# Performance work log

Hardware: AMD Instinct MI355X
Metric: run time of the kernel (lower is better)

## Reference

```python
import jax, jax.numpy as jnp
import numpy as np

TWN_THRESHOLD_FACTOR = 0.05
BN_EPS = 1e-5


def ternary_quantize(w):
    # threshold = 0.05 * max|w| (detached); q in {-1, 0, +1}
    t = TWN_THRESHOLD_FACTOR * jnp.max(jnp.abs(jax.lax.stop_gradient(w)))
    return (w > t).astype(w.dtype) - (w < -t).astype(w.dtype)


def conv2d(x, w, b):
    q = ternary_quantize(w)
    y = jax.lax.conv_general_dilated(x, q, (1, 1), 'VALID',
                                     dimension_numbers=('NCHW', 'OIHW', 'NCHW'))
    return y + b[None, :, None, None]


def linear(x, w, b):
    q = ternary_quantize(w)
    return x @ q.T + b


def bn_train(x, gamma, beta, axes):
    # training-mode batch norm (biased variance), matches torch BN in train()
    mean = jnp.mean(x, axis=axes, keepdims=True)
    var = jnp.var(x, axis=axes, keepdims=True)
    xhat = (x - mean) * jax.lax.rsqrt(var + BN_EPS)
    shape = [1] * x.ndim
    shape[1] = x.shape[1]
    return xhat * gamma.reshape(shape) + beta.reshape(shape)


def maxpool2(x):
    return jax.lax.reduce_window(x, -jnp.inf, jax.lax.max,
                                 (1, 1, 2, 2), (1, 1, 2, 2), 'VALID')


def setup_inputs() -> dict:
    key = jax.random.key(0)
    ks = jax.random.split(key, 8)
    B, Cin, H, W = 512, 1, 28, 28
    C1, C2, K = 64, 128, 5
    FLAT, F1, F2 = 4 * 4 * C2, 512, 10
    inp = {
        'x': jax.random.normal(ks[0], (B, Cin, H, W), jnp.float32),
        'conv1_w': jax.random.normal(ks[1], (C1, Cin, K, K), jnp.float32) * (1.0 / np.sqrt(Cin * K * K)),
        'conv1_b': jax.random.normal(ks[2], (C1,), jnp.float32) * 0.05,
        'bn1_g': jnp.ones((C1,), jnp.float32),
        'bn1_b': jnp.zeros((C1,), jnp.float32),
        'conv2_w': jax.random.normal(ks[3], (C2, C1, K, K), jnp.float32) * (1.0 / np.sqrt(C1 * K * K)),
        'conv2_b': jax.random.normal(ks[4], (C2,), jnp.float32) * 0.05,
        'bn2_g': jnp.ones((C2,), jnp.float32),
        'bn2_b': jnp.zeros((C2,), jnp.float32),
        'fc1_w': jax.random.normal(ks[5], (F1, FLAT), jnp.float32) * (1.0 / np.sqrt(FLAT)),
        'fc1_b': jax.random.normal(ks[6], (F1,), jnp.float32) * 0.05,
        'bn3_g': jnp.ones((F1,), jnp.float32),
        'bn3_b': jnp.zeros((F1,), jnp.float32),
        'fc2_w': jax.random.normal(ks[7], (F2, F1), jnp.float32) * (1.0 / np.sqrt(F1)),
        'fc2_b': jnp.zeros((F2,), jnp.float32),
    }
    return inp


def reference(x, conv1_w, conv1_b, bn1_g, bn1_b, conv2_w, conv2_b, bn2_g, bn2_b,
              fc1_w, fc1_b, bn3_g, bn3_b, fc2_w, fc2_b):
    h = jax.nn.relu(bn_train(conv2d(x, conv1_w, conv1_b), bn1_g, bn1_b, (0, 2, 3)))
    h = maxpool2(h)  # [B, 64, 12, 12]
    h = jax.nn.relu(bn_train(conv2d(h, conv2_w, conv2_b), bn2_g, bn2_b, (0, 2, 3)))
    h = maxpool2(h)  # [B, 128, 4, 4]
    h = h.reshape(h.shape[0], -1)  # [B, 2048]
    h = jax.nn.relu(bn_train(linear(h, fc1_w, fc1_b), bn3_g, bn3_b, (0,)))
    return linear(h, fc2_w, fc2_b)  # [B, 10]
```

## Files before the change

### kernel.cpp

```cpp
#include <hip/hip_runtime.h>
#include <stdint.h>

#define EPS 1e-5f

typedef short v8s __attribute__((ext_vector_type(8)));
typedef float v4f __attribute__((ext_vector_type(4)));

static const size_t W1F  = 4096;
static const size_t W2F  = 8192;
static const size_t WF2F = 212992;
static const size_t A_F  = 262144;
static const size_t B_F  = 19136512;
static const size_t WF1T = B_F + 1048576;

__device__ inline unsigned short f2bf(float f) {
    unsigned u = __float_as_uint(f);
    return (unsigned short)((u + 0x7FFF + ((u >> 16) & 1)) >> 16);
}

__device__ __forceinline__ void stage16(const unsigned short* g, unsigned short* l) {
    __builtin_amdgcn_global_load_lds(
        (const __attribute__((address_space(1))) unsigned int*)g,
        (__attribute__((address_space(3))) unsigned int*)l, 16, 0, 0);
}

__global__ void k_zero(float* p, int n) {
    int i = blockIdx.x * blockDim.x + threadIdx.x;
    if (i < n) p[i] = 0.f;
}

__global__ void k_absmax4(const float* __restrict__ w0, int n0,
                          const float* __restrict__ w1, int n1,
                          const float* __restrict__ w2, int n2,
                          const float* __restrict__ w3, int n3,
                          float* outv) {
    int blk = blockIdx.x;
    const float* w; int n; unsigned* out; int nb; int bi;
    if (blk < 1)        { w = w0; n = n0; out = (unsigned*)(outv + 0); nb = 1;   bi = blk;      }
    else if (blk < 17)  { w = w1; n = n1; out = (unsigned*)(outv + 1); nb = 16;  bi = blk - 1;  }
    else if (blk < 209) { w = w2; n = n2; out = (unsigned*)(outv + 2); nb = 192; bi = blk - 17; }
    else                { w = w3; n = n3; out = (unsigned*)(outv + 3); nb = 1;   bi = blk - 209; }
    float m = 0.f;
    for (int i = bi * 256 + threadIdx.x; i < n; i += nb * 256)
        m = fmaxf(m, fabsf(w[i]));
    #pragma unroll
    for (int o = 32; o; o >>= 1) m = fmaxf(m, __shfl_down(m, o));
    if ((threadIdx.x & 63) == 0) atomicMax(out, __float_as_uint(m));
}

__global__ void k_quantE(const float* __restrict__ c1w, const float* __restrict__ c2w,
                         const float* __restrict__ f2w, const float* __restrict__ am,
                         float* __restrict__ w1t, unsigned short* __restrict__ w2u,
                         float* __restrict__ wf2) {
    int blk = blockIdx.x;
    if (blk < 1) {
        float t = 0.05f * am[0];
        for (int i = threadIdx.x; i < 1600; i += 256) {
            float v = c1w[i];
            float q = (float)((v > t) - (v < -t));
            int c = i / 25, k = i - c * 25;
            w1t[k * 64 + c] = q;
        }
    } else if (blk < 401) {
        float t = 0.05f * am[1];
        int base = (blk - 1) * 512;
        #pragma unroll
        for (int jj = 0; jj < 2; ++jj) {
            int i = base + jj * 256 + threadIdx.x;
            int j    = i & 7;
            int lane = (i >> 3) & 63;
            int mt   = (i >> 9) & 7;
            int ks   = (i >> 12) & 1;
            int p    = i >> 13;
            int c  = mt * 16 + (lane & 15);
            int ci = ks * 32 + (lane >> 4) * 8 + j;
            float v = c2w[c * 1600 + ci * 25 + p];
            w2u[i] = (v > t) ? (unsigned short)0x3F80
                             : ((v < -t) ? (unsigned short)0xBF80 : (unsigned short)0);
        }
    } else {
        float t = 0.05f * am[3];
        for (int i = threadIdx.x; i < 5120; i += 256) {
            float v = f2w[i];
            wf2[i] = (float)((v > t) - (v < -t));
        }
    }
}

__global__ __launch_bounds__(512) void k_conv1(const float* __restrict__ x,
                                               const float* __restrict__ w1t,
                                               unsigned* __restrict__ pmn1,
                                               float* __restrict__ sum,
                                               float* __restrict__ ssq) {
    __shared__ float xs[784];
    __shared__ float red[2][8][64];
    int b = blockIdx.x;
    const float4* xim = (const float4*)(x + (size_t)b * 784);
    for (int i = threadIdx.x; i < 196; i += 512) ((float4*)xs)[i] = xim[i];
    int c  = threadIdx.x & 63;
    int wv = threadIdx.x >> 6;
    float w[25];
    #pragma unroll
    for (int k = 0; k < 25; ++k) w[k] = w1t[k * 64 + c];
    __syncthreads();
    unsigned* ob = pmn1 + (size_t)b * 9216;
    float s = 0.f, s2 = 0.f;
    int ph = 0, pw = wv;
    for (int it = 0; it < 18; ++it) {
        const float* xp = xs + (ph * 2) * 28 + pw * 2;
        float win[36];
        #pragma unroll
        for (int i = 0; i < 6; ++i)
            #pragma unroll
            for (int j = 0; j < 3; ++j) {
                float2 t2 = *(const float2*)(xp + i * 28 + j * 2);
                win[i * 6 + j * 2] = t2.x; win[i * 6 + j * 2 + 1] = t2.y;
            }
        float v00 = 0.f, v01 = 0.f, v10 = 0.f, v11 = 0.f;
        #pragma unroll
        for (int i = 0; i < 5; ++i)
            #pragma unroll
            for (int j = 0; j < 5; ++j) {
                float wk = w[i * 5 + j];
                v00 = fmaf(win[i * 6 + j],           wk, v00);
                v01 = fmaf(win[i * 6 + j + 1],       wk, v01);
                v10 = fmaf(win[(i + 1) * 6 + j],     wk, v10);
                v11 = fmaf(win[(i + 1) * 6 + j + 1], wk, v11);
            }
        s  += v00 + v01 + v10 + v11;
        s2 += v00 * v00 + v01 * v01 + v10 * v10 + v11 * v11;
        float mx = fmaxf(fmaxf(v00, v01), fmaxf(v10, v11));
        float mn = fminf(fminf(v00, v01), fminf(v10, v11));
        ob[(ph * 12 + pw) * 64 + c] = ((unsigned)f2bf(mx) << 16) | (unsigned)f2bf(mn);
        pw += 8; if (pw >= 12) { pw -= 12; ++ph; }
    }
    red[0][wv][c] = s; red[1][wv][c] = s2;
    __syncthreads();
    if (threadIdx.x < 64) {
        float S = 0.f, S2 = 0.f;
        #pragma unroll
        for (int i = 0; i < 8; ++i) { S += red[0][i][threadIdx.x]; S2 += red[1][i][threadIdx.x]; }
        atomicAdd(&sum[threadIdx.x], S);
        atomicAdd(&ssq[threadIdx.x], S2);
    }
}

__global__ void k_bnpool1(const unsigned* __restrict__ pmn1,
                          const float* __restrict__ c1sum, const float* __restrict__ c1ssq,
                          const float* __restrict__ g1, const float* __restrict__ b1,
                          unsigned short* __restrict__ pool1) {
    int i = blockIdx.x * 256 + threadIdx.x;
    int c = i & 63;
    const float invN = 1.f / 294912.f;
    float mean = c1sum[c] * invN;
    float var  = c1ssq[c] * invN - mean * mean;
    float sc = g1[c] * rsqrtf(var + EPS);
    float sh = b1[c] - mean * sc;
    unsigned u = pmn1[i];
    float mx = __uint_as_float(u & 0xffff0000u);
    float mn = __uint_as_float(u << 16);
    float v = (sc > 0.f) ? mx : mn;
    pool1[i] = f2bf(fmaxf(0.f, fmaf(v, sc, sh)));
}

__global__ __launch_bounds__(256) void k_conv2(const unsigned short* __restrict__ pool1,
                                               const unsigned short* __restrict__ wfrag,
                                               float* __restrict__ pmn,
                                               float* __restrict__ sum,
                                               float* __restrict__ ssq) {
    __shared__ unsigned short xs[144 * 76];
    __shared__ unsigned short wb[2][4096];
    __shared__ float reds[2][64], redq[2][64];
    int b     = blockIdx.x >> 1;
    int mhalf = blockIdx.x & 1;
    int tid  = threadIdx.x;
    int lane = tid & 63;
    int wave = tid >> 6;
    int nh = wave & 1, kp = wave >> 1;
    const unsigned short* src = pool1 + (size_t)b * 9216;
    for (int i = tid; i < 1152; i += 256) {
        int r = i >> 3, part = i & 7;
        *(float4*)(&xs[r * 76 + part * 8]) = *(const float4*)(src + r * 64 + part * 8);
    }
    #pragma unroll
    for (int h = 0; h < 2; ++h) {
        int ksm = wave * 2 + h;
        int ks = ksm >> 2, mt = ksm & 3;
        const unsigned short* g = wfrag + (size_t)(ks * 8 + mhalf * 4 + mt) * 512 + lane * 8;
        stage16(g, &wb[0][ks * 2048 + mt * 512 + lane * 8]);
    }
    __syncthreads();

    int n = lane & 15, quad = lane >> 4;
    int ow = n & 7;
    int ohb0 = nh * 4 + (n >> 3);
    int col0 = kp * 32 + quad * 8;
    v4f acc[4][2];
    #pragma unroll
    for (int mm = 0; mm < 4; ++mm) { acc[mm][0] = (v4f){0,0,0,0}; acc[mm][1] = (v4f){0,0,0,0}; }
    for (int p = 0; p < 25; ++p) {
        int cur = p & 1;
        if (p < 24) {
            #pragma unroll
            for (int h = 0; h < 2; ++h) {
                int ksm = wave * 2 + h;
                int ks = ksm >> 2, mt = ksm & 3;
                const unsigned short* g = wfrag +
                    (size_t)(((p + 1) * 2 + ks) * 8 + mhalf * 4 + mt) * 512 + lane * 8;
                stage16(g, &wb[cur ^ 1][ks * 2048 + mt * 512 + lane * 8]);
            }
        }
        int kh = p / 5, kw = p - (p / 5) * 5;
        int col = (ow + kw) * 76 + col0;
        v8s bf0 = *(const v8s*)(&xs[(ohb0 + kh) * 912 + col]);
        v8s bf1 = *(const v8s*)(&xs[(ohb0 + 2 + kh) * 912 + col]);
        #pragma unroll
        for (int mm = 0; mm < 4; ++mm) {
            v8s af = *(const v8s*)(&wb[cur][kp * 2048 + mm * 512 + lane * 8]);
            acc[mm][0] = __builtin_amdgcn_mfma_f32_16x16x32_bf16(af, bf0, acc[mm][0], 0, 0, 0);
            acc[mm][1] = __builtin_amdgcn_mfma_f32_16x16x32_bf16(af, bf1, acc[mm][1], 0, 0, 0);
        }
        __syncthreads();
    }
    float* mbuf = (float*)xs;
    if (kp == 1) {
        float* d = mbuf + (nh * 64 + lane) * 36;
        #pragma unroll
        for (int mm = 0; mm < 4; ++mm) {
            *(v4f*)(d + mm * 8)     = acc[mm][0];
            *(v4f*)(d + mm * 8 + 4) = acc[mm][1];
        }
    }
    __syncthreads();
    if (kp == 0) {
        const float* s = mbuf + (nh * 64 + lane) * 36;
        #pragma unroll
        for (int mm = 0; mm < 4; ++mm) {
            acc[mm][0] += *(const v4f*)(s + mm * 8);
            acc[mm][1] += *(const v4f*)(s + mm * 8 + 4);
        }
        float* po = pmn + (size_t)b * 4096;
        #pragma unroll
        for (int mm = 0; mm < 4; ++mm) {
            int cl0 = mm * 16 + quad * 4;
            #pragma unroll
            for (int r = 0; r < 4; ++r) {
                int cl = cl0 + r;
                int c  = mhalf * 64 + cl;
                float sA = 0.f, s2A = 0.f;
                #pragma unroll
                for (int bf = 0; bf < 2; ++bf) {
                    float v = acc[mm][bf][r];
                    float pm = fmaxf(v, __shfl_xor(v, 1));
                    float pn = fminf(v, __shfl_xor(v, 1));
                    pm = fmaxf(pm, __shfl_xor(pm, 8));
                    pn = fminf(pn, __shfl_xor(pn, 8));
                    if (((n & 1) == 0) && (n < 8)) {
                        int psp = (nh * 2 + bf) * 4 + (n >> 1);
                        *(float2*)(&po[(c * 16 + psp) * 2]) = make_float2(pm, pn);
                    }
                    float s = v, s2 = v * v;
                    #pragma unroll
                    for (int m = 1; m < 16; m <<= 1) { s += __shfl_xor(s, m); s2 += __shfl_xor(s2, m); }
                    sA += s; s2A += s2;
                }
                if (n == 0) { reds[nh][cl] = sA; redq[nh][cl] = s2A; }
            }
        }
    }
    __syncthreads();
    if (tid < 64) {
        atomicAdd(&sum[mhalf * 64 + tid], reds[0][tid] + reds[1][tid]);
        atomicAdd(&ssq[mhalf * 64 + tid], redq[0][tid] + redq[1][tid]);
    }
}

__global__ void k_prep_fc1(const float* __restrict__ w, const float* __restrict__ am,
                           unsigned short* __restrict__ wf,
                           const float* __restrict__ pmn2, const float* __restrict__ c2sum,
                           const float* __restrict__ c2ssq, const float* __restrict__ g2,
                           const float* __restrict__ b2, unsigned short* __restrict__ xfrag) {
    if (blockIdx.x < 4096) {
        float t = 0.05f * am[2];
        int i = blockIdx.x * 256 + threadIdx.x;
        int f = i >> 11, k = i & 2047;
        float v = w[i];
        unsigned short q = (v > t) ? (unsigned short)0x3F80
                         : ((v < -t) ? (unsigned short)0xBF80 : (unsigned short)0);
        int ft = f >> 4, fm = f & 15;
        int ks = k >> 5, kr = k & 31;
        int lane = (kr >> 3) * 16 + fm;
        wf[((size_t)(ks * 32 + ft) * 64 + lane) * 8 + (kr & 7)] = q;
    } else {
        int i = (blockIdx.x - 4096) * 256 + threadIdx.x;
        int j    = i & 7;
        int lane = (i >> 3) & 63;
        int bt   = (i >> 9) & 31;
        int ks   = i >> 14;
        int b = bt * 16 + (lane & 15);
        int k = ks * 32 + (lane >> 4) * 8 + j;
        int c = k >> 4, psp = k & 15;
        float2 mm = *(const float2*)(&pmn2[((size_t)b * 2048 + c * 16 + psp) * 2]);
        float mean = c2sum[c] * (1.f / 32768.f);
        float var  = c2ssq[c] * (1.f / 32768.f) - mean * mean;
        float sc = g2[c] * rsqrtf(var + EPS);
        float sh = b2[c] - mean * sc;
        float v = (sc > 0.f) ? mm.x : mm.y;
        xfrag[i] = f2bf(fmaxf(0.f, fmaf(v, sc, sh)));
    }
}

__global__ __launch_bounds__(256) void k_fc1(const unsigned short* __restrict__ xfrag,
                                             const unsigned short* __restrict__ wfrag,
                                             float* __restrict__ out,
                                             float* __restrict__ sum,
                                             float* __restrict__ ssq) {
    int lane = threadIdx.x & 63;
    int wave = threadIdx.x >> 6;
    int ft = (blockIdx.x & 7) * 4 + wave;
    int bT = blockIdx.x >> 3;
    v4f acc = (v4f){0.f, 0.f, 0.f, 0.f};
    for (int ks = 0; ks < 64; ++ks) {
        v8s bfrag = *(const v8s*)(xfrag + ((size_t)(ks * 32 + bT) * 64 + lane) * 8);
        v8s afrag = *(const v8s*)(wfrag + ((size_t)(ks * 32 + ft) * 64 + lane) * 8);
        acc = __builtin_amdgcn_mfma_f32_16x16x32_bf16(afrag, bfrag, acc, 0, 0, 0);
    }
    int bb = bT * 16 + (lane & 15);
    int quad = lane >> 4;
    int f0 = ft * 16 + quad * 4;
    *(float4*)(&out[(size_t)bb * 512 + f0]) =
        make_float4(acc[0], acc[1], acc[2], acc[3]);
    #pragma unroll
    for (int r = 0; r < 4; ++r) {
        float s = acc[r], s2 = s * s;
        #pragma unroll
        for (int m = 1; m < 16; m <<= 1) { s += __shfl_xor(s, m); s2 += __shfl_xor(s2, m); }
        if ((lane & 15) == 0) { atomicAdd(&sum[f0 + r], s); atomicAdd(&ssq[f0 + r], s2); }
    }
}

__global__ __launch_bounds__(256) void k_fc2(const float* __restrict__ x,
                                             const float* __restrict__ w,
                                             const float* __restrict__ bias,
                                             const float* __restrict__ fsum,
                                             const float* __restrict__ fssq,
                                             const float* __restrict__ g3,
                                             const float* __restrict__ b3,
                                             float* __restrict__ out) {
    int lane = threadIdx.x & 63;
    int b = blockIdx.x * 4 + (threadIdx.x >> 6);
    float xa[8], sm[8], sq[8], ga[8], ba[8];
    {
        const float4* p;
        p = (const float4*)(x + (size_t)b * 512 + lane * 8);
        *(float4*)xa = p[0]; *(float4*)(xa + 4) = p[1];
        p = (const float4*)(fsum + lane * 8);
        *(float4*)sm = p[0]; *(float4*)(sm + 4) = p[1];
        p = (const float4*)(fssq + lane * 8);
        *(float4*)sq = p[0]; *(float4*)(sq + 4) = p[1];
        p = (const float4*)(g3 + lane * 8);
        *(float4*)ga = p[0]; *(float4*)(ga + 4) = p[1];
        p = (const float4*)(b3 + lane * 8);
        *(float4*)ba = p[0]; *(float4*)(ba + 4) = p[1];
    }
    float h[8];
    #pragma unroll
    for (int e = 0; e < 8; ++e) {
        float mean = sm[e] * (1.f / 512.f);
        float var  = sq[e] * (1.f / 512.f) - mean * mean;
        float sc = ga[e] * rsqrtf(var + EPS);
        float sh = ba[e] - mean * sc;
        h[e] = fmaxf(0.f, fmaf(xa[e], sc, sh));
    }
    #pragma unroll
    for (int j = 0; j < 10; ++j) {
        const float4* wp = (const float4*)(w + j * 512 + lane * 8);
        float4 w0 = wp[0], w1 = wp[1];
        float p = h[0] * w0.x + h[1] * w0.y + h[2] * w0.z + h[3] * w0.w
                + h[4] * w1.x + h[5] * w1.y + h[6] * w1.z + h[7] * w1.w;
        #pragma unroll
        for (int o = 32; o; o >>= 1) p += __shfl_down(p, o);
        if (lane == 0) out[b * 10 + j] = p + bias[j];
    }
}

extern "C" void kernel_launch(void* const* d_in, const int* in_sizes, int n_in,
                              void* d_out, int out_size, void* d_ws, size_t ws_size,
                              hipStream_t stream) {
    const float* x       = (const float*)d_in[0];
    const float* conv1_w = (const float*)d_in[1];
    const float* bn1_g   = (const float*)d_in[3];
    const float* bn1_b   = (const float*)d_in[4];
    const float* conv2_w = (const float*)d_in[5];
    const float* bn2_g   = (const float*)d_in[7];
    const float* bn2_b   = (const float*)d_in[8];
    const float* fc1_w   = (const float*)d_in[9];
    const float* bn3_g   = (const float*)d_in[11];
    const float* bn3_b   = (const float*)d_in[12];
    const float* fc2_w   = (const float*)d_in[13];
    const float* fc2_b   = (const float*)d_in[14];

    float* wsf = (float*)d_ws;

    float* c1_sum = wsf + 16,   * c1_ssq = wsf + 80;
    float* c2_sum = wsf + 272,  * c2_ssq = wsf + 400;
    float* f_sum  = wsf + 1808, * f_ssq  = wsf + 2320;

    float* w1t = wsf + W1F;
    unsigned short* w2u = (unsigned short*)(wsf + W2F);
    float* wf2 = wsf + WF2F;
    unsigned short* wf1 = (unsigned short*)(wsf + WF1T);
    unsigned* PMN1 = (unsigned*)(wsf + A_F);
    float* PMN2 = wsf + A_F;
    float* A    = wsf + A_F;
    unsigned short* pool1 = (unsigned short*)(wsf + B_F);
    unsigned short* xfrag = (unsigned short*)(wsf + B_F);

    k_zero<<<16, 256, 0, stream>>>(wsf, 4096);

    k_absmax4<<<210, 256, 0, stream>>>(conv1_w, 1600, conv2_w, 204800,
                                       fc1_w, 1048576, fc2_w, 5120, wsf);

    k_quantE<<<402, 256, 0, stream>>>(conv1_w, conv2_w, fc2_w, wsf, w1t, w2u, wf2);

    k_conv1<<<512, 512, 0, stream>>>(x, w1t, PMN1, c1_sum, c1_ssq);

    k_bnpool1<<<18432, 256, 0, stream>>>(PMN1, c1_sum, c1_ssq, bn1_g, bn1_b, pool1);

    k_conv2<<<1024, 256, 0, stream>>>(pool1, w2u, PMN2, c2_sum, c2_ssq);

    k_prep_fc1<<<8192, 256, 0, stream>>>(fc1_w, wsf, wf1, PMN2, c2_sum, c2_ssq,
                                         bn2_g, bn2_b, xfrag);

    k_fc1<<<256, 256, 0, stream>>>(xfrag, wf1, A, f_sum, f_ssq);

    k_fc2<<<128, 256, 0, stream>>>(A, wf2, fc2_b, f_sum, f_ssq, bn3_g, bn3_b,
                                   (float*)d_out);
}
```

Before: 210.4 us.

## Fuse pipeline into three cooperative kernels with grid-wide syncs

Replaces nine kernel launches with three cooperative kernels: front (zero, absmax, quantize, conv1, BN1+pool), conv2 (conv2 MFMA plus BN2 and fc1 input prep) and back (fc1 plus BN3 and fc2). Grid syncs stand in for launch boundaries, conv1 max/min results stay in registers across the BN1 sync, and fc1 weight quantization moves into the front kernel. This targets launch overhead and intermediate global round trips. The cost is that all blocks must be co-resident, and work is redistributed over a fixed grid, which may lower parallelism in some phases. The old kernels remain as fallbacks if a cooperative launch fails.

```diff
diff --git a/kernel.cpp b/kernel.cpp
--- a/kernel.cpp
+++ b/kernel.cpp
@@ -1,5 +1,8 @@
 #include <hip/hip_runtime.h>
+#include <hip/hip_cooperative_groups.h>
 #include <stdint.h>
+
+namespace cg = cooperative_groups;
 
 #define EPS 1e-5f
 
@@ -10,8 +13,8 @@
 static const size_t W2F  = 8192;
 static const size_t WF2F = 212992;
 static const size_t A_F  = 262144;
+static const size_t WF1N = 2359296;
 static const size_t B_F  = 19136512;
-static const size_t WF1T = B_F + 1048576;
 
 __device__ inline unsigned short f2bf(float f) {
     unsigned u = __float_as_uint(f);
@@ -23,6 +26,398 @@
         (const __attribute__((address_space(1))) unsigned int*)g,
         (__attribute__((address_space(3))) unsigned int*)l, 16, 0, 0);
 }
+
+
+__global__ __launch_bounds__(512, 2) void k_front(
+    const float* __restrict__ x, const float* __restrict__ c1w,
+    const float* __restrict__ c2w, const float* __restrict__ f1w,
+    const float* __restrict__ f2w, const float* __restrict__ g1,
+    const float* __restrict__ b1, float* wsf)
+{
+    __shared__ float xs[784];
+    __shared__ float red[2][8][64];
+    cg::grid_group grid = cg::this_grid();
+    int tid = threadIdx.x;
+    int blk = blockIdx.x;
+
+    float* am     = wsf;
+    float* c1_sum = wsf + 16;
+    float* c1_ssq = wsf + 80;
+    float* w1t = wsf + W1F;
+    unsigned short* w2u = (unsigned short*)(wsf + W2F);
+    float* wf2 = wsf + WF2F;
+    unsigned short* wf1 = (unsigned short*)(wsf + WF1N);
+    unsigned short* pool1 = (unsigned short*)(wsf + B_F);
+
+    if (blk < 8) wsf[blk * 512 + tid] = 0.f;
+    __threadfence();
+    grid.sync();
+    __threadfence();
+
+    {
+        const float* w; int n; unsigned* out; int nb; int bi;
+        if (blk == 0)      { w = c1w; n = 1600;    out = (unsigned*)(am + 0); nb = 1;   bi = 0; }
+        else if (blk == 1) { w = f2w; n = 5120;    out = (unsigned*)(am + 3); nb = 1;   bi = 0; }
+        else if (blk < 66) { w = c2w; n = 204800;  out = (unsigned*)(am + 1); nb = 64;  bi = blk - 2; }
+        else               { w = f1w; n = 1048576; out = (unsigned*)(am + 2); nb = 190; bi = blk - 66; }
+        float m = 0.f;
+        for (int i = bi * 512 + tid; i < n; i += nb * 512)
+            m = fmaxf(m, fabsf(w[i]));
+        #pragma unroll
+        for (int o = 32; o; o >>= 1) m = fmaxf(m, __shfl_down(m, o));
+        if ((tid & 63) == 0) atomicMax(out, __float_as_uint(m));
+    }
+    __threadfence();
+    grid.sync();
+    __threadfence();
+
+    if (blk == 0) {
+        float t = 0.05f * am[0];
+        for (int i = tid; i < 1600; i += 512) {
+            float v = c1w[i];
+            float q = (float)((v > t) - (v < -t));
+            int c = i / 25, k = i - c * 25;
+            w1t[k * 64 + c] = q;
+        }
+    } else if (blk == 1) {
+        float t = 0.05f * am[3];
+        for (int i = tid; i < 5120; i += 512) {
+            float v = f2w[i];
+            wf2[i] = (float)((v > t) - (v < -t));
+        }
+    } else if (blk < 42) {
+        float t = 0.05f * am[1];
+        for (int i = (blk - 2) * 512 + tid; i < 204800; i += 40 * 512) {
+            int j    = i & 7;
+            int lane = (i >> 3) & 63;
+            int mt   = (i >> 9) & 7;
+            int ks   = (i >> 12) & 1;
+            int p    = i >> 13;
+            int c  = mt * 16 + (lane & 15);
+            int ci = ks * 32 + (lane >> 4) * 8 + j;
+            float v = c2w[c * 1600 + ci * 25 + p];
+            w2u[i] = (v > t) ? (unsigned short)0x3F80
+                             : ((v < -t) ? (unsigned short)0xBF80 : (unsigned short)0);
+        }
+    } else {
+        float t = 0.05f * am[2];
+        for (int i = (blk - 42) * 512 + tid; i < 1048576; i += 214 * 512) {
+            float v = f1w[i];
+            unsigned short q = (v > t) ? (unsigned short)0x3F80
+                             : ((v < -t) ? (unsigned short)0xBF80 : (unsigned short)0);
+            int f = i >> 11, k = i & 2047;
+            int ft = f >> 4, fm = f & 15;
+            int ks = k >> 5, kr = k & 31;
+            int lane = (kr >> 3) * 16 + fm;
+            wf1[((size_t)(ks * 32 + ft) * 64 + lane) * 8 + (kr & 7)] = q;
+        }
+    }
+    __threadfence();
+    grid.sync();
+    __threadfence();
+
+    int c  = tid & 63;
+    int wv = tid >> 6;
+    unsigned pmnR0[18], pmnR1[18];
+    float w[25];
+    #pragma unroll
+    for (int k = 0; k < 25; ++k) w[k] = w1t[k * 64 + c];
+    float s = 0.f, s2 = 0.f;
+
+    auto conv_img = [&](int b, unsigned* pmnR) {
+        __syncthreads();
+        const float4* xim = (const float4*)(x + (size_t)b * 784);
+        for (int i = tid; i < 196; i += 512) ((float4*)xs)[i] = xim[i];
+        __syncthreads();
+        int ph = 0, pw = wv;
+        #pragma unroll
+        for (int it = 0; it < 18; ++it) {
+            const float* xp = xs + (ph * 2) * 28 + pw * 2;
+            float win[36];
+            #pragma unroll
+            for (int i = 0; i < 6; ++i)
+                #pragma unroll
+                for (int j = 0; j < 3; ++j) {
+                    float2 t2 = *(const float2*)(xp + i * 28 + j * 2);
+                    win[i * 6 + j * 2] = t2.x; win[i * 6 + j * 2 + 1] = t2.y;
+                }
+            float v00 = 0.f, v01 = 0.f, v10 = 0.f, v11 = 0.f;
+            #pragma unroll
+            for (int i = 0; i < 5; ++i)
+                #pragma unroll
+                for (int j = 0; j < 5; ++j) {
+                    float wk = w[i * 5 + j];
+                    v00 = fmaf(win[i * 6 + j],           wk, v00);
+                    v01 = fmaf(win[i * 6 + j + 1],       wk, v01);
+                    v10 = fmaf(win[(i + 1) * 6 + j],     wk, v10);
+                    v11 = fmaf(win[(i + 1) * 6 + j + 1], wk, v11);
+                }
+            s  += v00 + v01 + v10 + v11;
+            s2 += v00 * v00 + v01 * v01 + v10 * v10 + v11 * v11;
+            float mx = fmaxf(fmaxf(v00, v01), fmaxf(v10, v11));
+            float mn = fminf(fminf(v00, v01), fminf(v10, v11));
+            pmnR[it] = ((unsigned)f2bf(mx) << 16) | (unsigned)f2bf(mn);
+            pw += 8; if (pw >= 12) { pw -= 12; ++ph; }
+        }
+    };
+    conv_img(blk,       pmnR0);
+    conv_img(blk + 256, pmnR1);
+
+    red[0][wv][c] = s; red[1][wv][c] = s2;
+    __syncthreads();
+    if (tid < 64) {
+        float S = 0.f, S2 = 0.f;
+        #pragma unroll
+        for (int i = 0; i < 8; ++i) { S += red[0][i][tid]; S2 += red[1][i][tid]; }
+        atomicAdd(&c1_sum[tid], S);
+        atomicAdd(&c1_ssq[tid], S2);
+    }
+    __threadfence();
+    grid.sync();
+    __threadfence();
+
+    {
+        const float invN = 1.f / 294912.f;
+        float mean = c1_sum[c] * invN;
+        float var  = c1_ssq[c] * invN - mean * mean;
+        float sc = g1[c] * rsqrtf(var + EPS);
+        float sh = b1[c] - mean * sc;
+        auto fin_img = [&](int b, const unsigned* pmnR) {
+            unsigned short* ob = pool1 + (size_t)b * 9216;
+            #pragma unroll
+            for (int it = 0; it < 18; ++it) {
+                int pos = it * 8 + wv;
+                unsigned u = pmnR[it];
+                float mx = __uint_as_float(u & 0xffff0000u);
+                float mn = __uint_as_float(u << 16);
+                float v = (sc > 0.f) ? mx : mn;
+                ob[pos * 64 + c] = f2bf(fmaxf(0.f, fmaf(v, sc, sh)));
+            }
+        };
+        fin_img(blk,       pmnR0);
+        fin_img(blk + 256, pmnR1);
+    }
+}
+
+__global__ __launch_bounds__(256, 2) void k_conv2f(
+    const unsigned short* pool1, const unsigned short* __restrict__ wfrag,
+    const float* __restrict__ g2, const float* __restrict__ b2, float* wsf)
+{
+    __shared__ unsigned short xs[144 * 76];
+    __shared__ unsigned short wb[2][4096];
+    __shared__ float reds[2][64], redq[2][64];
+    cg::grid_group grid = cg::this_grid();
+
+    float* c2_sum = wsf + 272;
+    float* c2_ssq = wsf + 400;
+    float* pmnG   = wsf + A_F;
+    unsigned short* xfrag = (unsigned short*)(wsf + B_F);
+
+    int tid  = threadIdx.x;
+    int lane = tid & 63;
+    int wave = tid >> 6;
+    int nh = wave & 1, kp = wave >> 1;
+    int n = lane & 15, quad = lane >> 4;
+    int ow = n & 7;
+    int ohb0 = nh * 4 + (n >> 3);
+    int col0 = kp * 32 + quad * 8;
+
+    #pragma unroll
+    for (int t = 0; t < 2; ++t) {
+        int tile  = (int)blockIdx.x + t * 512;
+        int img   = tile >> 1;
+        int mhalf = tile & 1;
+        const unsigned short* src = pool1 + (size_t)img * 9216;
+        __syncthreads();
+        for (int i = tid; i < 1152; i += 256) {
+            int r = i >> 3, part = i & 7;
+            *(float4*)(&xs[r * 76 + part * 8]) = *(const float4*)(src + r * 64 + part * 8);
+        }
+        #pragma unroll
+        for (int h = 0; h < 2; ++h) {
+            int ksm = wave * 2 + h;
+            int ks = ksm >> 2, mt = ksm & 3;
+            stage16(wfrag + (size_t)(ks * 8 + mhalf * 4 + mt) * 512 + lane * 8,
+                    &wb[0][ks * 2048 + mt * 512 + lane * 8]);
+        }
+        __syncthreads();
+
+        v4f acc[4][2];
+        #pragma unroll
+        for (int mm = 0; mm < 4; ++mm) { acc[mm][0] = (v4f){0,0,0,0}; acc[mm][1] = (v4f){0,0,0,0}; }
+        for (int p = 0; p < 25; ++p) {
+            int cur = p & 1;
+            if (p < 24) {
+                #pragma unroll
+                for (int h = 0; h < 2; ++h) {
+                    int ksm = wave * 2 + h;
+                    int ks = ksm >> 2, mt = ksm & 3;
+                    stage16(wfrag + (size_t)(((p + 1) * 2 + ks) * 8 + mhalf * 4 + mt) * 512 + lane * 8,
+                            &wb[cur ^ 1][ks * 2048 + mt * 512 + lane * 8]);
+                }
+            }
+            int kh = p / 5, kw = p - (p / 5) * 5;
+            int col = (ow + kw) * 76 + col0;
+            v8s bf0 = *(const v8s*)(&xs[(ohb0 + kh) * 912 + col]);
+            v8s bf1 = *(const v8s*)(&xs[(ohb0 + 2 + kh) * 912 + col]);
+            #pragma unroll
+            for (int mm = 0; mm < 4; ++mm) {
+                v8s af = *(const v8s*)(&wb[cur][kp * 2048 + mm * 512 + lane * 8]);
+                acc[mm][0] = __builtin_amdgcn_mfma_f32_16x16x32_bf16(af, bf0, acc[mm][0], 0, 0, 0);
+                acc[mm][1] = __builtin_amdgcn_mfma_f32_16x16x32_bf16(af, bf1, acc[mm][1], 0, 0, 0);
+            }
+            __syncthreads();
+        }
+        float* mbuf = (float*)xs;
+        if (kp == 1) {
+            float* d = mbuf + (nh * 64 + lane) * 36;
+            #pragma unroll
+            for (int mm = 0; mm < 4; ++mm) {
+                *(v4f*)(d + mm * 8)     = acc[mm][0];
+                *(v4f*)(d + mm * 8 + 4) = acc[mm][1];
+            }
+        }
+        __syncthreads();
+        if (kp == 0) {
+            const float* ms = mbuf + (nh * 64 + lane) * 36;
+            #pragma unroll
+            for (int mm = 0; mm < 4; ++mm) {
+                acc[mm][0] += *(const v4f*)(ms + mm * 8);
+                acc[mm][1] += *(const v4f*)(ms + mm * 8 + 4);
+            }
+            float* po = pmnG + (size_t)img * 4096;
+            #pragma unroll
+            for (int mm = 0; mm < 4; ++mm) {
+                int cl0 = mm * 16 + quad * 4;
+                #pragma unroll
+                for (int r = 0; r < 4; ++r) {
+                    int cl = cl0 + r;
+                    int cc = mhalf * 64 + cl;
+                    float sA = 0.f, s2A = 0.f;
+                    #pragma unroll
+                    for (int bf = 0; bf < 2; ++bf) {
+                        float v = acc[mm][bf][r];
+                        float pm = fmaxf(v, __shfl_xor(v, 1));
+                        float pn = fminf(v, __shfl_xor(v, 1));
+                        pm = fmaxf(pm, __shfl_xor(pm, 8));
+                        pn = fminf(pn, __shfl_xor(pn, 8));
+                        if (((n & 1) == 0) && (n < 8)) {
+                            int psp = (nh * 2 + bf) * 4 + (n >> 1);
+                            *(float2*)(&po[(cc * 16 + psp) * 2]) = make_float2(pm, pn);
+                        }
+                        float s = v, s2 = v * v;
+                        #pragma unroll
+                        for (int m = 1; m < 16; m <<= 1) { s += __shfl_xor(s, m); s2 += __shfl_xor(s2, m); }
+                        sA += s; s2A += s2;
+                    }
+                    if (n == 0) { reds[nh][cl] = sA; redq[nh][cl] = s2A; }
+                }
+            }
+        }
+        __syncthreads();
+        if (tid < 64) {
+            atomicAdd(&c2_sum[mhalf * 64 + tid], reds[0][tid] + reds[1][tid]);
+            atomicAdd(&c2_ssq[mhalf * 64 + tid], redq[0][tid] + redq[1][tid]);
+        }
+    }
+    __threadfence();
+    grid.sync();
+    __threadfence();
+    for (int i = (int)blockIdx.x * 256 + tid; i < 1048576; i += 512 * 256) {
+        int j    = i & 7;
+        int lw   = (i >> 3) & 63;
+        int bt   = (i >> 9) & 31;
+        int ks   = i >> 14;
+        int b = bt * 16 + (lw & 15);
+        int k = ks * 32 + (lw >> 4) * 8 + j;
+        int cc = k >> 4, psp = k & 15;
+        float2 mm2 = *(const float2*)(&pmnG[((size_t)b * 2048 + cc * 16 + psp) * 2]);
+        float mean = c2_sum[cc] * (1.f / 32768.f);
+        float var  = c2_ssq[cc] * (1.f / 32768.f) - mean * mean;
+        float sc = g2[cc] * rsqrtf(var + EPS);
+        float sh = b2[cc] - mean * sc;
+        float v = (sc > 0.f) ? mm2.x : mm2.y;
+        xfrag[i] = f2bf(fmaxf(0.f, fmaf(v, sc, sh)));
+    }
+}
+
+__global__ __launch_bounds__(256) void k_back(
+    const float* __restrict__ bias2, const float* __restrict__ g3,
+    const float* __restrict__ b3, float* __restrict__ out, float* wsf)
+{
+    cg::grid_group grid = cg::this_grid();
+    const unsigned short* xfrag = (const unsigned short*)(wsf + B_F);
+    const unsigned short* wfrag = (const unsigned short*)(wsf + WF1N);
+    float* A     = wsf + A_F;
+    float* f_sum = wsf + 1808;
+    float* f_ssq = wsf + 2320;
+    const float* wf2 = wsf + WF2F;
+
+    int lane = threadIdx.x & 63;
+    int wave = threadIdx.x >> 6;
+    {
+        int ft = (blockIdx.x & 7) * 4 + wave;
+        int bT = blockIdx.x >> 3;
+        v4f acc = (v4f){0.f, 0.f, 0.f, 0.f};
+        for (int ks = 0; ks < 64; ++ks) {
+            v8s bfrag = *(const v8s*)(xfrag + ((size_t)(ks * 32 + bT) * 64 + lane) * 8);
+            v8s afrag = *(const v8s*)(wfrag + ((size_t)(ks * 32 + ft) * 64 + lane) * 8);
+            acc = __builtin_amdgcn_mfma_f32_16x16x32_bf16(afrag, bfrag, acc, 0, 0, 0);
+        }
+        int bb = bT * 16 + (lane & 15);
+        int quad = lane >> 4;
+        int f0 = ft * 16 + quad * 4;
+        *(float4*)(&A[(size_t)bb * 512 + f0]) =
+            make_float4(acc[0], acc[1], acc[2], acc[3]);
+        #pragma unroll
+        for (int r = 0; r < 4; ++r) {
+            float s = acc[r], s2 = s * s;
+            #pragma unroll
+            for (int m = 1; m < 16; m <<= 1) { s += __shfl_xor(s, m); s2 += __shfl_xor(s2, m); }
+            if ((lane & 15) == 0) { atomicAdd(&f_sum[f0 + r], s); atomicAdd(&f_ssq[f0 + r], s2); }
+        }
+    }
+    __threadfence();
+    grid.sync();
+    __threadfence();
+    if (blockIdx.x < 128) {
+        int b = blockIdx.x * 4 + wave;
+        float xa[8], sm[8], sq[8], ga[8], ba[8];
+        {
+            const float4* p;
+            p = (const float4*)(A + (size_t)b * 512 + lane * 8);
+            *(float4*)xa = p[0]; *(float4*)(xa + 4) = p[1];
+            p = (const float4*)(f_sum + lane * 8);
+            *(float4*)sm = p[0]; *(float4*)(sm + 4) = p[1];
+            p = (const float4*)(f_ssq + lane * 8);
+            *(float4*)sq = p[0]; *(float4*)(sq + 4) = p[1];
+            p = (const float4*)(g3 + lane * 8);
+            *(float4*)ga = p[0]; *(float4*)(ga + 4) = p[1];
+            p = (const float4*)(b3 + lane * 8);
+            *(float4*)ba = p[0]; *(float4*)(ba + 4) = p[1];
+        }
+        float h[8];
+        #pragma unroll
+        for (int e = 0; e < 8; ++e) {
+            float mean = sm[e] * (1.f / 512.f);
+            float var  = sq[e] * (1.f / 512.f) - mean * mean;
+            float sc = ga[e] * rsqrtf(var + EPS);
+            float sh = ba[e] - mean * sc;
+            h[e] = fmaxf(0.f, fmaf(xa[e], sc, sh));
+        }
+        #pragma unroll
+        for (int j = 0; j < 10; ++j) {
+            const float4* wp = (const float4*)(wf2 + j * 512 + lane * 8);
+            float4 w0 = wp[0], w1 = wp[1];
+            float p = h[0] * w0.x + h[1] * w0.y + h[2] * w0.z + h[3] * w0.w
+                    + h[4] * w1.x + h[5] * w1.y + h[6] * w1.z + h[7] * w1.w;
+            #pragma unroll
+            for (int o = 32; o; o >>= 1) p += __shfl_down(p, o);
+            if (lane == 0) out[b * 10 + j] = p + bias2[j];
+        }
+    }
+}
+
 
 __global__ void k_zero(float* p, int n) {
     int i = blockIdx.x * blockDim.x + threadIdx.x;
@@ -400,40 +795,69 @@
     const float* fc2_w   = (const float*)d_in[13];
     const float* fc2_b   = (const float*)d_in[14];
 
-    float* wsf = (float*)d_ws;
+    float* wsf  = (float*)d_ws;
+    float* outp = (float*)d_out;
 
     float* c1_sum = wsf + 16,   * c1_ssq = wsf + 80;
     float* c2_sum = wsf + 272,  * c2_ssq = wsf + 400;
     float* f_sum  = wsf + 1808, * f_ssq  = wsf + 2320;
-
     float* w1t = wsf + W1F;
     unsigned short* w2u = (unsigned short*)(wsf + W2F);
     float* wf2 = wsf + WF2F;
-    unsigned short* wf1 = (unsigned short*)(wsf + WF1T);
+    unsigned short* wf1 = (unsigned short*)(wsf + WF1N);
     unsigned* PMN1 = (unsigned*)(wsf + A_F);
     float* PMN2 = wsf + A_F;
     float* A    = wsf + A_F;
     unsigned short* pool1 = (unsigned short*)(wsf + B_F);
     unsigned short* xfrag = (unsigned short*)(wsf + B_F);
 
-    k_zero<<<16, 256, 0, stream>>>(wsf, 4096);
-
-    k_absmax4<<<210, 256, 0, stream>>>(conv1_w, 1600, conv2_w, 204800,
-                                       fc1_w, 1048576, fc2_w, 5120, wsf);
-
-    k_quantE<<<402, 256, 0, stream>>>(conv1_w, conv2_w, fc2_w, wsf, w1t, w2u, wf2);
-
-    k_conv1<<<512, 512, 0, stream>>>(x, w1t, PMN1, c1_sum, c1_ssq);
-
-    k_bnpool1<<<18432, 256, 0, stream>>>(PMN1, c1_sum, c1_ssq, bn1_g, bn1_b, pool1);
-
-    k_conv2<<<1024, 256, 0, stream>>>(pool1, w2u, PMN2, c2_sum, c2_ssq);
-
-    k_prep_fc1<<<8192, 256, 0, stream>>>(fc1_w, wsf, wf1, PMN2, c2_sum, c2_ssq,
-                                         bn2_g, bn2_b, xfrag);
-
-    k_fc1<<<256, 256, 0, stream>>>(xfrag, wf1, A, f_sum, f_ssq);
-
-    k_fc2<<<128, 256, 0, stream>>>(A, wf2, fc2_b, f_sum, f_ssq, bn3_g, bn3_b,
-                                   (float*)d_out);
-}
+    const unsigned short* pool1c = pool1;
+    const unsigned short* w2uc   = w2u;
+
+    bool ok1;
+    {
+        void* args[] = {(void*)&x, (void*)&conv1_w, (void*)&conv2_w, (void*)&fc1_w,
+                        (void*)&fc2_w, (void*)&bn1_g, (void*)&bn1_b, (void*)&wsf};
+        ok1 = hipLaunchCooperativeKernel((void*)k_front, dim3(256), dim3(512),
+                                         args, 0, stream) == hipSuccess;
+    }
+    if (!ok1) {
+        k_zero<<<16, 256, 0, stream>>>(wsf, 4096);
+        k_absmax4<<<210, 256, 0, stream>>>(conv1_w, 1600, conv2_w, 204800,
+                                           fc1_w, 1048576, fc2_w, 5120, wsf);
+        k_quantE<<<402, 256, 0, stream>>>(conv1_w, conv2_w, fc2_w, wsf, w1t, w2u, wf2);
+        k_conv1<<<512, 512, 0, stream>>>(x, w1t, PMN1, c1_sum, c1_ssq);
+        k_bnpool1<<<18432, 256, 0, stream>>>(PMN1, c1_sum, c1_ssq, bn1_g, bn1_b, pool1);
+        k_conv2<<<1024, 256, 0, stream>>>(pool1, w2u, PMN2, c2_sum, c2_ssq);
+        k_prep_fc1<<<8192, 256, 0, stream>>>(fc1_w, wsf, wf1, PMN2, c2_sum, c2_ssq,
+                                             bn2_g, bn2_b, xfrag);
+        k_fc1<<<256, 256, 0, stream>>>(xfrag, wf1, A, f_sum, f_ssq);
+        k_fc2<<<128, 256, 0, stream>>>(A, wf2, fc2_b, f_sum, f_ssq, bn3_g, bn3_b, outp);
+        return;
+    }
+
+    bool ok2;
+    {
+        void* args[] = {(void*)&pool1c, (void*)&w2uc, (void*)&bn2_g, (void*)&bn2_b,
+                        (void*)&wsf};
+        ok2 = hipLaunchCooperativeKernel((void*)k_conv2f, dim3(512), dim3(256),
+                                         args, 0, stream) == hipSuccess;
+    }
+    if (!ok2) {
+        k_conv2<<<1024, 256, 0, stream>>>(pool1, w2u, PMN2, c2_sum, c2_ssq);
+        k_prep_fc1<<<8192, 256, 0, stream>>>(fc1_w, wsf, wf1, PMN2, c2_sum, c2_ssq,
+                                             bn2_g, bn2_b, xfrag);
+    }
+
+    bool ok3;
+    {
+        void* args[] = {(void*)&fc2_b, (void*)&bn3_g, (void*)&bn3_b, (void*)&outp,
+                        (void*)&wsf};
+        ok3 = hipLaunchCooperativeKernel((void*)k_back, dim3(256), dim3(256),
+                                         args, 0, stream) == hipSuccess;
+    }
+    if (!ok3) {
+        k_fc1<<<256, 256, 0, stream>>>(xfrag, wf1, A, f_sum, f_ssq);
+        k_fc2<<<128, 256, 0, stream>>>(A, wf2, fc2_b, f_sum, f_ssq, bn3_g, bn3_b, outp);
+    }
+}
```

Result: slower. 802.5 us (+281.3%).
